# Optimization experiments

Hardware: AMD Instinct MI355X
Metric: run time of the kernel (lower is better)

Reference implementation:

```python
import jax, jax.numpy as jnp
import numpy as np

TEMPERATURE = 0.1
NEG_INF = -1e9
EPS = 1e-12

def setup_inputs() -> dict:
    key = jax.random.key(0)
    k1, k2, k3 = jax.random.split(key, 3)
    B, C, H, W = 8, 256, 128, 128
    num_classes = 150
    features = jax.random.normal(k1, (B, C, H, W), dtype=jnp.float32)
    labels = jax.random.randint(k2, (B, H, W), 0, num_classes, dtype=jnp.int32)
    text_embeddings = jax.random.normal(k3, (num_classes, C), dtype=jnp.float32)
    return {"features": features, "labels": labels, "text_embeddings": text_embeddings, "ignore_index": 255}

def _l2_normalize(x, axis=-1):
    n = jnp.linalg.norm(x, axis=axis, keepdims=True)
    return x / jnp.maximum(n, EPS)

def reference(features, labels, text_embeddings, ignore_index):
    num_classes, C = text_embeddings.shape
    B = features.shape[0]
    # [B,C,H,W] -> [B*H*W, C]
    f = jnp.transpose(features, (0, 2, 3, 1)).reshape(-1, C)
    lab = jnp.where(labels == ignore_index, 0, labels).reshape(-1)
    # segment-mean per class (fused scatter-add instead of per-class loop)
    sums = jax.ops.segment_sum(f, lab, num_segments=num_classes)          # [K,C]
    counts = jax.ops.segment_sum(jnp.ones_like(lab, dtype=f.dtype), lab, num_segments=num_classes)  # [K]
    valid = counts > 0
    prototypes = jnp.where(valid[:, None], sums / jnp.maximum(counts, 1.0)[:, None], 0.0)
    prototypes = _l2_normalize(prototypes)
    text_n = _l2_normalize(text_embeddings)
    sim = (prototypes @ text_n.T) / TEMPERATURE                            # [K,K]
    # cross-entropy restricted to valid rows/cols with identity soft targets
    masked = jnp.where(valid[None, :], sim, NEG_INF)                       # mask invalid cols
    logp = jax.nn.log_softmax(masked, axis=-1)
    diag = jnp.diagonal(logp)
    per_row = jnp.where(valid, -diag, 0.0)
    n_valid = jnp.sum(valid.astype(f.dtype))
    loss = jnp.sum(per_row) / jnp.maximum(n_valid, 1.0)
    return jnp.where(n_valid > 1, loss, 0.0)
```

## Files before the change

### kernel.cpp

```cpp
#include <hip/hip_runtime.h>
#include <math.h>

#define EPSV 1e-12f

typedef __attribute__((ext_vector_type(8))) short short8;
typedef __attribute__((ext_vector_type(4))) float f32x4;

constexpr int MT    = 10;
constexpr int K_PAD = MT * 16;
constexpr int CPB   = 64;
constexpr int CHUNK = 128;
constexpr int PBPX  = 2048;
constexpr int NCHK  = PBPX / CHUNK;
constexpr int NPB   = 64;
constexpr int THR   = 512;
constexpr int LROW  = 136;

__device__ __forceinline__ unsigned short f2bf(float f) {
    unsigned u = __builtin_bit_cast(unsigned, f);
    return (unsigned short)((u + 0x7FFFu + ((u >> 16) & 1u)) >> 16);
}

__global__ __launch_bounds__(THR) void protomm_kernel(
    const float* __restrict__ feat,
    const int*   __restrict__ labels,
    const int*   __restrict__ ign_p,
    float*       __restrict__ partial,
    float*       __restrict__ vmask,
    int C, int HW)
{
    __shared__ unsigned short Bf[2][CPB * LROW];
    __shared__ int   labL[2][CHUNK];
    __shared__ float fscr[4][K_PAD * 16];
    __shared__ unsigned char pres[K_PAD];

    const int tid   = threadIdx.x;
    const int w     = tid >> 6;
    const int l     = tid & 63;
    const int ct    = w & 3;
    const int kh    = w >> 2;
    const int rowid = l & 15;
    const int g     = l >> 4;

    const int bid = blockIdx.x;
    const int cg  = bid & 3;
    const int pb  = bid >> 2;
    const int b   = pb >> 3;
    const int px0 = (pb & 7) * PBPX;
    const int ig  = *ign_p;

    const int q   = tid & 31;
    const int chp = tid >> 5;
    const float* fb = feat + ((size_t)(b * C + cg * CPB + chp)) * HW + px0 + 4 * q;
    const int*   lb = labels + (size_t)b * HW + px0;

    if (cg == 0)
        for (int i = tid; i < K_PAD; i += THR) pres[i] = 0;

    f32x4 acc[MT];
    #pragma unroll
    for (int m = 0; m < MT; ++m) acc[m] = (f32x4){0.f, 0.f, 0.f, 0.f};

    float4 pf0, pf1, pf2, pf3;
    int4   plab;
    auto issue = [&](int ck) {
        const float* p = fb + ck * CHUNK;
        pf0 = *reinterpret_cast<const float4*>(p);
        pf1 = *reinterpret_cast<const float4*>(p + (size_t)16 * HW);
        pf2 = *reinterpret_cast<const float4*>(p + (size_t)32 * HW);
        pf3 = *reinterpret_cast<const float4*>(p + (size_t)48 * HW);
        if (tid < 32)
            plab = *reinterpret_cast<const int4*>(lb + ck * CHUNK + 4 * tid);
    };
    auto commit = [&](int buf) {
        float4 v[4] = {pf0, pf1, pf2, pf3};
        #pragma unroll
        for (int i = 0; i < 4; ++i) {
            unsigned* dst = reinterpret_cast<unsigned*>(
                &Bf[buf][(chp + 16 * i) * LROW + 4 * q]);
            dst[0] = (unsigned)f2bf(v[i].x) | ((unsigned)f2bf(v[i].y) << 16);
            dst[1] = (unsigned)f2bf(v[i].z) | ((unsigned)f2bf(v[i].w) << 16);
        }
        if (tid < 32) {
            int4 lv = plab;
            lv.x = (lv.x == ig) ? 0 : lv.x;
            lv.y = (lv.y == ig) ? 0 : lv.y;
            lv.z = (lv.z == ig) ? 0 : lv.z;
            lv.w = (lv.w == ig) ? 0 : lv.w;
            *reinterpret_cast<int4*>(&labL[buf][4 * tid]) = lv;
        }
    };

    issue(0);

    for (int ck = 0; ck < NCHK; ++ck) {
        const int cur = ck & 1;
        commit(cur);
        if (ck + 1 < NCHK) issue(ck + 1);
        __syncthreads();

        if (cg == 0 && tid < CHUNK) {
            int la = labL[cur][tid];
            if ((unsigned)la < (unsigned)K_PAD) pres[la] = 1;
        }

        #pragma unroll
        for (int kk = 0; kk < 2; ++kk) {
            const int ks = 2 * kh + kk;
            const int* lp = &labL[cur][ks * 32 + g * 8];
            const int la0 = lp[0], la1 = lp[1], la2 = lp[2], la3 = lp[3];
            const int la4 = lp[4], la5 = lp[5], la6 = lp[6], la7 = lp[7];
            const short8 bfrag = *reinterpret_cast<const short8*>(
                &Bf[cur][(ct * 16 + rowid) * LROW + ks * 32 + g * 8]);
            #pragma unroll
            for (int m = 0; m < MT; ++m) {
                const int tgt = m * 16 + rowid;
                unsigned w0 = (la0 == tgt ? 0x3F80u : 0u) | (la1 == tgt ? 0x3F800000u : 0u);
                unsigned w1 = (la2 == tgt ? 0x3F80u : 0u) | (la3 == tgt ? 0x3F800000u : 0u);
                unsigned w2 = (la4 == tgt ? 0x3F80u : 0u) | (la5 == tgt ? 0x3F800000u : 0u);
                unsigned w3 = (la6 == tgt ? 0x3F80u : 0u) | (la7 == tgt ? 0x3F800000u : 0u);
                uint4 aw = make_uint4(w0, w1, w2, w3);
                short8 afrag = __builtin_bit_cast(short8, aw);
                acc[m] = __builtin_amdgcn_mfma_f32_16x16x32_bf16(afrag, bfrag, acc[m], 0, 0, 0);
            }
        }
    }

    __syncthreads();
    if (kh == 1) {
        #pragma unroll
        for (int m = 0; m < MT; ++m)
            #pragma unroll
            for (int r = 0; r < 4; ++r)
                fscr[ct][(m * 16 + g * 4 + r) * 16 + rowid] = acc[m][r];
    }
    __syncthreads();
    if (kh == 0) {
        float* dst = partial + (size_t)pb * K_PAD * C + cg * CPB + ct * 16 + rowid;
        #pragma unroll
        for (int m = 0; m < MT; ++m)
            #pragma unroll
            for (int r = 0; r < 4; ++r) {
                const int cls = m * 16 + g * 4 + r;
                dst[(size_t)cls * C] = acc[m][r] + fscr[ct][cls * 16 + rowid];
            }
    }
    if (cg == 0) {
        for (int i = tid; i < K_PAD; i += THR)
            if (pres[i]) vmask[i] = 1.0f;
    }
}

__global__ __launch_bounds__(256) void tail_kernel(
    const float* __restrict__ partial,
    const float* __restrict__ text,
    const float* __restrict__ vmask,
    float* __restrict__ loss_acc,
    unsigned int* __restrict__ ticket,
    float* __restrict__ out,
    int K, int C, int nblocks)
{
    __shared__ float ph[256];
    __shared__ float vm[K_PAD];
    __shared__ float red[5];
    __shared__ float wred[12];
    __shared__ unsigned int lastflag;

    const int k    = blockIdx.x;
    const int tid  = threadIdx.x;
    const int wid  = tid >> 6;
    const int lane = tid & 63;

    if (tid < K_PAD) vm[tid] = vmask[tid];
    __syncthreads();
    const bool valid = (vm[k] > 0.f);

    float contrib = 0.f;
    if (valid) {
        const size_t gs = (size_t)K_PAD * C;
        const float* pp = partial + (size_t)k * C + tid;
        float a0 = 0.f, a1 = 0.f, a2 = 0.f, a3 = 0.f;
        float a4 = 0.f, a5 = 0.f, a6 = 0.f, a7 = 0.f;
        for (int g = 0; g < NPB; g += 8) {
            a0 += pp[(g + 0) * gs]; a1 += pp[(g + 1) * gs];
            a2 += pp[(g + 2) * gs]; a3 += pp[(g + 3) * gs];
            a4 += pp[(g + 4) * gs]; a5 += pp[(g + 5) * gs];
            a6 += pp[(g + 6) * gs]; a7 += pp[(g + 7) * gs];
        }
        float sums = (((a0 + a1) + (a2 + a3)) + ((a4 + a5) + (a6 + a7)));

        float v = sums * sums;
        #pragma unroll
        for (int o = 32; o > 0; o >>= 1) v += __shfl_down(v, o);
        if (lane == 0) red[wid] = v;
        __syncthreads();
        if (tid == 0) {
            float s = red[0] + red[1] + red[2] + red[3];
            red[4] = 1.0f / fmaxf(sqrtf(s), EPSV);
        }
        __syncthreads();
        ph[tid] = sums * red[4];
        __syncthreads();

        float m = -INFINITY, s = 0.f, skk = 0.f;
        #pragma unroll 1
        for (int gq = 0; gq < K_PAD / 16; ++gq) {
            const int j0 = gq * 16 + wid * 4;
            const float* t0 = text + (size_t)(j0 + 0 < K ? j0 + 0 : K - 1) * C;
            const float* t1 = text + (size_t)(j0 + 1 < K ? j0 + 1 : K - 1) * C;
            const float* t2 = text + (size_t)(j0 + 2 < K ? j0 + 2 : K - 1) * C;
            const float* t3 = text + (size_t)(j0 + 3 < K ? j0 + 3 : K - 1) * C;
            float d0 = 0.f, d1 = 0.f, d2 = 0.f, d3 = 0.f;
            float q0 = 0.f, q1 = 0.f, q2 = 0.f, q3 = 0.f;
            #pragma unroll
            for (int cc = lane; cc < 256; cc += 64) {
                float p  = ph[cc];
                float x0 = t0[cc], x1 = t1[cc], x2 = t2[cc], x3 = t3[cc];
                d0 = fmaf(p, x0, d0);  q0 = fmaf(x0, x0, q0);
                d1 = fmaf(p, x1, d1);  q1 = fmaf(x1, x1, q1);
                d2 = fmaf(p, x2, d2);  q2 = fmaf(x2, x2, q2);
                d3 = fmaf(p, x3, d3);  q3 = fmaf(x3, x3, q3);
            }
            #pragma unroll
            for (int o = 32; o > 0; o >>= 1) {
                d0 += __shfl_down(d0, o); d1 += __shfl_down(d1, o);
                d2 += __shfl_down(d2, o); d3 += __shfl_down(d3, o);
                q0 += __shfl_down(q0, o); q1 += __shfl_down(q1, o);
                q2 += __shfl_down(q2, o); q3 += __shfl_down(q3, o);
            }
            if (lane == 0) {
                float dd[4] = {d0, d1, d2, d3};
                float qq[4] = {q0, q1, q2, q3};
                #pragma unroll
                for (int r = 0; r < 4; ++r) {
                    int j = j0 + r;
                    float vmj = vm[j];
                    float sim = dd[r] * (10.0f / fmaxf(sqrtf(qq[r]), EPSV));
                    float ms  = vmj * sim - (1.f - vmj) * 1e9f;
                    if (j == k) skk = ms;
                    if (ms > m) { s = s * expf(m - ms) + 1.f; m = ms; }
                    else        { s += expf(ms - m); }
                }
            }
        }
        if (lane == 0) { wred[wid*3+0] = m; wred[wid*3+1] = s; wred[wid*3+2] = skk; }
        __syncthreads();
        if (tid == 0) {
            float M = fmaxf(fmaxf(wred[0], wred[3]), fmaxf(wred[6], wred[9]));
            float S = 0.f, SKK = 0.f;
            #pragma unroll
            for (int ww = 0; ww < 4; ++ww) {
                S   += wred[ww*3+1] * expf(wred[ww*3+0] - M);
                SKK += wred[ww*3+2];
            }
            contrib = M + logf(S) - SKK;
        }
    }

    if (tid == 0) {
        if (valid) atomicAdd(loss_acc, contrib);
        __threadfence();
        unsigned old = atomicAdd(ticket, 1u);
        lastflag = (old == (unsigned)(nblocks - 1)) ? 1u : 0u;
    }
    __syncthreads();
    if (lastflag) {
        float v = (tid < K_PAD) ? vm[tid] : 0.f;
        #pragma unroll
        for (int o = 32; o > 0; o >>= 1) v += __shfl_down(v, o);
        if (lane == 0) red[wid] = v;
        __syncthreads();
        if (tid == 0) {
            float nv = red[0] + red[1] + red[2] + red[3];
            float total = atomicAdd(loss_acc, 0.0f);
            out[0] = (nv > 1.f) ? total / fmaxf(nv, 1.f) : 0.f;
        }
    }
}

extern "C" void kernel_launch(void* const* d_in, const int* in_sizes, int n_in,
                              void* d_out, int out_size, void* d_ws, size_t ws_size,
                              hipStream_t stream) {
    const float* feat   = (const float*)d_in[0];
    const int*   labels = (const int*)d_in[1];
    const float* text   = (const float*)d_in[2];
    const int*   ign    = (const int*)d_in[3];

    const int B  = 8;
    const int N  = in_sizes[1];
    const int HW = N / B;
    const int C  = in_sizes[0] / N;
    const int K  = in_sizes[2] / C;

    float*        partial  = (float*)d_ws;
    float*        vmask    = partial + (size_t)NPB * K_PAD * C;
    float*        loss_acc = vmask + K_PAD;
    unsigned int* ticket   = (unsigned int*)(loss_acc + 1);

    hipMemsetAsync(vmask, 0, (K_PAD + 2) * sizeof(float), stream);

    protomm_kernel<<<NPB * 4, THR, 0, stream>>>(
        feat, labels, ign, partial, vmask, C, HW);

    tail_kernel<<<K, 256, 0, stream>>>(
        partial, text, vmask, loss_acc, ticket, (float*)d_out, K, C, K);
}
```

Before: 69.96 us.

## Halve pixels per block, restructure MFMA tiling, vectorize tail reduction

The prototype kernel now uses 1024 pixels per block, which doubles the block count to 512 and the number of partial slabs to 128, and declares launch bounds for 4 blocks per CU. Each wave now owns class tiles across all four channel tiles, so one A fragment built from labels is reused over four B fragments, at the cost of a larger accumulator set. The tail kernel reduces partials with float4 loads split over four groups plus an LDS combine, vectorizes the text dot products, and switches to fast __expf. More partials raise the tail's read traffic and the register pressure may limit occupancy.

```diff
diff --git a/kernel.cpp b/kernel.cpp
--- a/kernel.cpp
+++ b/kernel.cpp
@@ -10,18 +10,19 @@
 constexpr int K_PAD = MT * 16;
 constexpr int CPB   = 64;
 constexpr int CHUNK = 128;
-constexpr int PBPX  = 2048;
+constexpr int PBPX  = 1024;
 constexpr int NCHK  = PBPX / CHUNK;
-constexpr int NPB   = 64;
+constexpr int NPB   = 128;
 constexpr int THR   = 512;
 constexpr int LROW  = 136;
+constexpr int FROW  = 68;
 
 __device__ __forceinline__ unsigned short f2bf(float f) {
     unsigned u = __builtin_bit_cast(unsigned, f);
     return (unsigned short)((u + 0x7FFFu + ((u >> 16) & 1u)) >> 16);
 }
 
-__global__ __launch_bounds__(THR) void protomm_kernel(
+__global__ __launch_bounds__(THR, 4) void protomm_kernel(
     const float* __restrict__ feat,
     const int*   __restrict__ labels,
     const int*   __restrict__ ign_p,
@@ -31,13 +32,13 @@
 {
     __shared__ unsigned short Bf[2][CPB * LROW];
     __shared__ int   labL[2][CHUNK];
-    __shared__ float fscr[4][K_PAD * 16];
+    __shared__ float fscr[K_PAD * FROW];
     __shared__ unsigned char pres[K_PAD];
 
     const int tid   = threadIdx.x;
     const int w     = tid >> 6;
     const int l     = tid & 63;
-    const int ct    = w & 3;
+    const int q     = w & 3;
     const int kh    = w >> 2;
     const int rowid = l & 15;
     const int g     = l >> 4;
@@ -45,21 +46,24 @@
     const int bid = blockIdx.x;
     const int cg  = bid & 3;
     const int pb  = bid >> 2;
-    const int b   = pb >> 3;
-    const int px0 = (pb & 7) * PBPX;
+    const int b   = pb >> 4;
+    const int px0 = (pb & 15) * PBPX;
     const int ig  = *ign_p;
 
-    const int q   = tid & 31;
+    const int qq  = tid & 31;
     const int chp = tid >> 5;
-    const float* fb = feat + ((size_t)(b * C + cg * CPB + chp)) * HW + px0 + 4 * q;
+    const float* fb = feat + ((size_t)(b * C + cg * CPB + chp)) * HW + px0 + 4 * qq;
     const int*   lb = labels + (size_t)b * HW + px0;
 
     if (cg == 0)
         for (int i = tid; i < K_PAD; i += THR) pres[i] = 0;
 
-    f32x4 acc[MT];
+    f32x4 acc[3][4];
     #pragma unroll
-    for (int m = 0; m < MT; ++m) acc[m] = (f32x4){0.f, 0.f, 0.f, 0.f};
+    for (int mi = 0; mi < 3; ++mi)
+        #pragma unroll
+        for (int ct = 0; ct < 4; ++ct)
+            acc[mi][ct] = (f32x4){0.f, 0.f, 0.f, 0.f};
 
     float4 pf0, pf1, pf2, pf3;
     int4   plab;
@@ -77,7 +81,7 @@
         #pragma unroll
         for (int i = 0; i < 4; ++i) {
             unsigned* dst = reinterpret_cast<unsigned*>(
-                &Bf[buf][(chp + 16 * i) * LROW + 4 * q]);
+                &Bf[buf][(chp + 16 * i) * LROW + 4 * qq]);
             dst[0] = (unsigned)f2bf(v[i].x) | ((unsigned)f2bf(v[i].y) << 16);
             dst[1] = (unsigned)f2bf(v[i].z) | ((unsigned)f2bf(v[i].w) << 16);
         }
@@ -107,21 +111,29 @@
         #pragma unroll
         for (int kk = 0; kk < 2; ++kk) {
             const int ks = 2 * kh + kk;
-            const int* lp = &labL[cur][ks * 32 + g * 8];
-            const int la0 = lp[0], la1 = lp[1], la2 = lp[2], la3 = lp[3];
-            const int la4 = lp[4], la5 = lp[5], la6 = lp[6], la7 = lp[7];
-            const short8 bfrag = *reinterpret_cast<const short8*>(
-                &Bf[cur][(ct * 16 + rowid) * LROW + ks * 32 + g * 8]);
+            const int4 lA = *reinterpret_cast<const int4*>(&labL[cur][ks * 32 + g * 8]);
+            const int4 lB = *reinterpret_cast<const int4*>(&labL[cur][ks * 32 + g * 8 + 4]);
+            short8 bfragv[4];
             #pragma unroll
-            for (int m = 0; m < MT; ++m) {
-                const int tgt = m * 16 + rowid;
-                unsigned w0 = (la0 == tgt ? 0x3F80u : 0u) | (la1 == tgt ? 0x3F800000u : 0u);
-                unsigned w1 = (la2 == tgt ? 0x3F80u : 0u) | (la3 == tgt ? 0x3F800000u : 0u);
-                unsigned w2 = (la4 == tgt ? 0x3F80u : 0u) | (la5 == tgt ? 0x3F800000u : 0u);
-                unsigned w3 = (la6 == tgt ? 0x3F80u : 0u) | (la7 == tgt ? 0x3F800000u : 0u);
-                uint4 aw = make_uint4(w0, w1, w2, w3);
-                short8 afrag = __builtin_bit_cast(short8, aw);
-                acc[m] = __builtin_amdgcn_mfma_f32_16x16x32_bf16(afrag, bfrag, acc[m], 0, 0, 0);
+            for (int ct = 0; ct < 4; ++ct)
+                bfragv[ct] = *reinterpret_cast<const short8*>(
+                    &Bf[cur][(ct * 16 + rowid) * LROW + ks * 32 + g * 8]);
+            #pragma unroll
+            for (int mi = 0; mi < 3; ++mi) {
+                const int m = q + 4 * mi;
+                if (m < MT) {
+                    const int tgt = m * 16 + rowid;
+                    unsigned w0 = (lA.x == tgt ? 0x3F80u : 0u) | (lA.y == tgt ? 0x3F800000u : 0u);
+                    unsigned w1 = (lA.z == tgt ? 0x3F80u : 0u) | (lA.w == tgt ? 0x3F800000u : 0u);
+                    unsigned w2 = (lB.x == tgt ? 0x3F80u : 0u) | (lB.y == tgt ? 0x3F800000u : 0u);
+                    unsigned w3 = (lB.z == tgt ? 0x3F80u : 0u) | (lB.w == tgt ? 0x3F800000u : 0u);
+                    uint4 aw = make_uint4(w0, w1, w2, w3);
+                    short8 afrag = __builtin_bit_cast(short8, aw);
+                    #pragma unroll
+                    for (int ct = 0; ct < 4; ++ct)
+                        acc[mi][ct] = __builtin_amdgcn_mfma_f32_16x16x32_bf16(
+                            afrag, bfragv[ct], acc[mi][ct], 0, 0, 0);
+                }
             }
         }
     }
@@ -129,21 +141,33 @@
     __syncthreads();
     if (kh == 1) {
         #pragma unroll
-        for (int m = 0; m < MT; ++m)
-            #pragma unroll
-            for (int r = 0; r < 4; ++r)
-                fscr[ct][(m * 16 + g * 4 + r) * 16 + rowid] = acc[m][r];
+        for (int mi = 0; mi < 3; ++mi) {
+            const int m = q + 4 * mi;
+            if (m < MT)
+                #pragma unroll
+                for (int ct = 0; ct < 4; ++ct)
+                    #pragma unroll
+                    for (int r = 0; r < 4; ++r)
+                        fscr[(m * 16 + g * 4 + r) * FROW + ct * 16 + rowid] = acc[mi][ct][r];
+        }
     }
     __syncthreads();
     if (kh == 0) {
-        float* dst = partial + (size_t)pb * K_PAD * C + cg * CPB + ct * 16 + rowid;
-        #pragma unroll
-        for (int m = 0; m < MT; ++m)
-            #pragma unroll
-            for (int r = 0; r < 4; ++r) {
-                const int cls = m * 16 + g * 4 + r;
-                dst[(size_t)cls * C] = acc[m][r] + fscr[ct][cls * 16 + rowid];
-            }
+        float* dst = partial + (size_t)pb * K_PAD * C + cg * CPB;
+        #pragma unroll
+        for (int mi = 0; mi < 3; ++mi) {
+            const int m = q + 4 * mi;
+            if (m < MT)
+                #pragma unroll
+                for (int ct = 0; ct < 4; ++ct)
+                    #pragma unroll
+                    for (int r = 0; r < 4; ++r) {
+                        const int cls = m * 16 + g * 4 + r;
+                        const int col = ct * 16 + rowid;
+                        dst[(size_t)cls * C + col] =
+                            acc[mi][ct][r] + fscr[cls * FROW + col];
+                    }
+        }
     }
     if (cg == 0) {
         for (int i = tid; i < K_PAD; i += THR)
@@ -161,6 +185,7 @@
     int K, int C, int nblocks)
 {
     __shared__ float ph[256];
+    __shared__ float scr[4][260];
     __shared__ float vm[K_PAD];
     __shared__ float red[5];
     __shared__ float wred[12];
@@ -177,19 +202,28 @@
 
     float contrib = 0.f;
     if (valid) {
+        const int cq = tid & 63;
+        const int sg = tid >> 6;
         const size_t gs = (size_t)K_PAD * C;
-        const float* pp = partial + (size_t)k * C + tid;
-        float a0 = 0.f, a1 = 0.f, a2 = 0.f, a3 = 0.f;
-        float a4 = 0.f, a5 = 0.f, a6 = 0.f, a7 = 0.f;
-        for (int g = 0; g < NPB; g += 8) {
-            a0 += pp[(g + 0) * gs]; a1 += pp[(g + 1) * gs];
-            a2 += pp[(g + 2) * gs]; a3 += pp[(g + 3) * gs];
-            a4 += pp[(g + 4) * gs]; a5 += pp[(g + 5) * gs];
-            a6 += pp[(g + 6) * gs]; a7 += pp[(g + 7) * gs];
-        }
-        float sums = (((a0 + a1) + (a2 + a3)) + ((a4 + a5) + (a6 + a7)));
-
-        float v = sums * sums;
+        const float* pbase = partial + (size_t)k * C + 4 * cq;
+        float4 a0 = {0,0,0,0}, a1 = {0,0,0,0}, a2 = {0,0,0,0}, a3 = {0,0,0,0};
+        float4 a4 = {0,0,0,0}, a5 = {0,0,0,0}, a6 = {0,0,0,0}, a7 = {0,0,0,0};
+        for (int s = sg; s < NPB; s += 32) {
+            a0 += *(const float4*)(pbase + (size_t)(s +  0) * gs);
+            a1 += *(const float4*)(pbase + (size_t)(s +  4) * gs);
+            a2 += *(const float4*)(pbase + (size_t)(s +  8) * gs);
+            a3 += *(const float4*)(pbase + (size_t)(s + 12) * gs);
+            a4 += *(const float4*)(pbase + (size_t)(s + 16) * gs);
+            a5 += *(const float4*)(pbase + (size_t)(s + 20) * gs);
+            a6 += *(const float4*)(pbase + (size_t)(s + 24) * gs);
+            a7 += *(const float4*)(pbase + (size_t)(s + 28) * gs);
+        }
+        float4 asum = (((a0 + a1) + (a2 + a3)) + ((a4 + a5) + (a6 + a7)));
+        *(float4*)&scr[sg][4 * cq] = asum;
+        __syncthreads();
+        float val = scr[0][tid] + scr[1][tid] + scr[2][tid] + scr[3][tid];
+
+        float v = val * val;
         #pragma unroll
         for (int o = 32; o > 0; o >>= 1) v += __shfl_down(v, o);
         if (lane == 0) red[wid] = v;
@@ -199,28 +233,27 @@
             red[4] = 1.0f / fmaxf(sqrtf(s), EPSV);
         }
         __syncthreads();
-        ph[tid] = sums * red[4];
-        __syncthreads();
-
+        ph[tid] = val * red[4];
+        __syncthreads();
+
+        const float4 pv = *(const float4*)&ph[4 * lane];
         float m = -INFINITY, s = 0.f, skk = 0.f;
         #pragma unroll 1
         for (int gq = 0; gq < K_PAD / 16; ++gq) {
             const int j0 = gq * 16 + wid * 4;
-            const float* t0 = text + (size_t)(j0 + 0 < K ? j0 + 0 : K - 1) * C;
-            const float* t1 = text + (size_t)(j0 + 1 < K ? j0 + 1 : K - 1) * C;
-            const float* t2 = text + (size_t)(j0 + 2 < K ? j0 + 2 : K - 1) * C;
-            const float* t3 = text + (size_t)(j0 + 3 < K ? j0 + 3 : K - 1) * C;
-            float d0 = 0.f, d1 = 0.f, d2 = 0.f, d3 = 0.f;
-            float q0 = 0.f, q1 = 0.f, q2 = 0.f, q3 = 0.f;
-            #pragma unroll
-            for (int cc = lane; cc < 256; cc += 64) {
-                float p  = ph[cc];
-                float x0 = t0[cc], x1 = t1[cc], x2 = t2[cc], x3 = t3[cc];
-                d0 = fmaf(p, x0, d0);  q0 = fmaf(x0, x0, q0);
-                d1 = fmaf(p, x1, d1);  q1 = fmaf(x1, x1, q1);
-                d2 = fmaf(p, x2, d2);  q2 = fmaf(x2, x2, q2);
-                d3 = fmaf(p, x3, d3);  q3 = fmaf(x3, x3, q3);
-            }
+            const float4* t0 = (const float4*)(text + (size_t)(j0 + 0 < K ? j0 + 0 : 0) * C);
+            const float4* t1 = (const float4*)(text + (size_t)(j0 + 1 < K ? j0 + 1 : 0) * C);
+            const float4* t2 = (const float4*)(text + (size_t)(j0 + 2 < K ? j0 + 2 : 0) * C);
+            const float4* t3 = (const float4*)(text + (size_t)(j0 + 3 < K ? j0 + 3 : 0) * C);
+            float4 x0 = t0[lane], x1 = t1[lane], x2 = t2[lane], x3 = t3[lane];
+            float d0 = pv.x*x0.x + pv.y*x0.y + pv.z*x0.z + pv.w*x0.w;
+            float q0 = x0.x*x0.x + x0.y*x0.y + x0.z*x0.z + x0.w*x0.w;
+            float d1 = pv.x*x1.x + pv.y*x1.y + pv.z*x1.z + pv.w*x1.w;
+            float q1 = x1.x*x1.x + x1.y*x1.y + x1.z*x1.z + x1.w*x1.w;
+            float d2 = pv.x*x2.x + pv.y*x2.y + pv.z*x2.z + pv.w*x2.w;
+            float q2 = x2.x*x2.x + x2.y*x2.y + x2.z*x2.z + x2.w*x2.w;
+            float d3 = pv.x*x3.x + pv.y*x3.y + pv.z*x3.z + pv.w*x3.w;
+            float q3 = x3.x*x3.x + x3.y*x3.y + x3.z*x3.z + x3.w*x3.w;
             #pragma unroll
             for (int o = 32; o > 0; o >>= 1) {
                 d0 += __shfl_down(d0, o); d1 += __shfl_down(d1, o);
@@ -234,12 +267,12 @@
                 #pragma unroll
                 for (int r = 0; r < 4; ++r) {
                     int j = j0 + r;
-                    float vmj = vm[j];
+                    float vmj = (j < K_PAD) ? vm[j] : 0.f;
                     float sim = dd[r] * (10.0f / fmaxf(sqrtf(qq[r]), EPSV));
                     float ms  = vmj * sim - (1.f - vmj) * 1e9f;
                     if (j == k) skk = ms;
-                    if (ms > m) { s = s * expf(m - ms) + 1.f; m = ms; }
-                    else        { s += expf(ms - m); }
+                    if (ms > m) { s = s * __expf(m - ms) + 1.f; m = ms; }
+                    else        { s += __expf(ms - m); }
                 }
             }
         }
@@ -250,7 +283,7 @@
             float S = 0.f, SKK = 0.f;
             #pragma unroll
             for (int ww = 0; ww < 4; ++ww) {
-                S   += wred[ww*3+1] * expf(wred[ww*3+0] - M);
+                S   += wred[ww*3+1] * __expf(wred[ww*3+0] - M);
                 SKK += wred[ww*3+2];
             }
             contrib = M + logf(S) - SKK;
```

Result: faster. 66.32 us (-5.2%).
